# Kernel tuning notes

Measured on AMD Instinct MI355X. Metric: run time of the kernel, lower is better.

Reference implementation:

```python
import jax, jax.numpy as jnp
import numpy as np

B, D, H, Z, E = 65536, 128, 256, 128, 16  # batch, input, hidden, hyper, embedding


def setup_inputs() -> dict:
    key = jax.random.key(0)
    ks = jax.random.split(key, 20)
    s = 0.02  # small weight scale for numerical sanity
    return {
        "x": jax.random.normal(ks[0], (B, D), jnp.float32),
        "h0": jax.random.normal(ks[1], (B, H), jnp.float32),
        "c0": jax.random.normal(ks[2], (B, H), jnp.float32),
        "hhat0": jax.random.normal(ks[3], (B, Z), jnp.float32),
        "chat0": jax.random.normal(ks[4], (B, Z), jnp.float32),
        "hweight": jax.random.normal(ks[5], (Z + H + D, 4 * Z), jnp.float32) * s,
        "hbias": jnp.zeros((4 * Z,), jnp.float32),
        "zw_h": jax.random.normal(ks[6], (Z, 4 * E), jnp.float32) * s,
        "zw_x": jax.random.normal(ks[7], (Z, 4 * E), jnp.float32) * s,
        "zw_b": jax.random.normal(ks[8], (Z, 4 * E), jnp.float32) * 0.01,
        "zb_h": jnp.ones((4 * E,), jnp.float32),
        "zb_x": jnp.ones((4 * E,), jnp.float32),
        "dw_h": jnp.full((4, E, H), 0.1 / E, jnp.float32),  # [i,g,f,o] stacked
        "dw_x": jnp.full((4, E, H), 0.1 / E, jnp.float32),
        "dw_b": jax.random.normal(ks[9], (4, E, H), jnp.float32) * s,
        "weight": jax.random.normal(ks[10], (H + D, 4 * H), jnp.float32) * s,
        "bias": jnp.zeros((4 * H,), jnp.float32),
    }


def reference(x, h0, c0, hhat0, chat0, hweight, hbias, zw_h, zw_x, zw_b,
              zb_h, zb_x, dw_h, dw_x, dw_b, weight, bias):
    sig, tanh = jax.nn.sigmoid, jnp.tanh
    b = x.shape[0]
    # hyper LSTM cell
    gh = jnp.concatenate([hhat0, h0, x], axis=1) @ hweight + hbias  # [B, 4Z]
    i_h, g_h, f_h, o_h = jnp.split(gh, 4, axis=1)
    chat1 = sig(f_h) * chat0 + sig(i_h) * tanh(g_h)
    hhat1 = sig(o_h) * tanh(chat1)
    # embedding projections z (chunk order i,g,f,o -> reshape to [B,4,E])
    z_h = (hhat1 @ zw_h + zb_h).reshape(b, 4, E)
    z_x = (hhat1 @ zw_x + zb_x).reshape(b, 4, E)
    z_b = (hhat1 @ zw_b).reshape(b, 4, E)
    # d scaling vectors, [B,4,H] -> [B,4H]
    d_yh = jnp.einsum('bke,keh->bkh', z_h, dw_h).reshape(b, 4 * H)
    d_yx = jnp.einsum('bke,keh->bkh', z_x, dw_x).reshape(b, 4 * H)
    d_yb = jnp.einsum('bke,keh->bkh', z_b, dw_b).reshape(b, 4 * H)
    # main LSTM gates, hyper-modulated
    g = jnp.concatenate([h0, x], axis=1) @ weight * d_yh * d_yx + d_yb + bias
    i_g, g_g, f_g, o_g = jnp.split(g, 4, axis=1)
    c1 = sig(f_g) * c0 + sig(i_g) * tanh(g_g)
    h1 = sig(o_g) * tanh(c1)
    return (h1, c1, hhat1, chat1)
```

## Files before the change

kernel.cpp:

```cpp
#include <hip/hip_runtime.h>


typedef unsigned short u16;
typedef __attribute__((ext_vector_type(8))) short bf16x8;
typedef __attribute__((ext_vector_type(4))) float f32x4;

#define BATCH 65536

__device__ __forceinline__ u16 f2b(float f) {
  unsigned u = __float_as_uint(f);
  u += 0x7fffu + ((u >> 16) & 1u);
  return (u16)(u >> 16);
}
__device__ __forceinline__ unsigned pk2(float a, float b) {
  return (unsigned)f2b(a) | ((unsigned)f2b(b) << 16);
}
__device__ __forceinline__ float upk_lo(unsigned u) { return __uint_as_float(u << 16); }
__device__ __forceinline__ float upk_hi(unsigned u) { return __uint_as_float(u & 0xffff0000u); }
__device__ __forceinline__ float sigf(float x) { return 1.0f / (1.0f + __expf(-x)); }
__device__ __forceinline__ float tanhfast(float x) {
  float xc = fminf(fmaxf(x, -15.f), 15.f);
  float e = __expf(2.f * xc);
  return (e - 1.f) / (e + 1.f);
}
__device__ __forceinline__ int swz(int r, int c) { return r * 64 + (c ^ ((r & 7) << 3)); }

#define VM_BAR(N) do { \
  asm volatile("s_waitcnt vmcnt(" #N ")" ::: "memory"); \
  __builtin_amdgcn_s_barrier(); \
  __builtin_amdgcn_sched_barrier(0); } while (0)

__device__ __forceinline__ void gl_lds16(const u16* g, u16* l) {
  __builtin_amdgcn_global_load_lds(
      (const __attribute__((address_space(1))) void*)g,
      (__attribute__((address_space(3))) void*)l, 16, 0, 0);
}
__device__ __forceinline__ void stageA(const u16* base, int ldk, u16* lA, int t) {
  const int r = t >> 3, q = t & 7, wid = t >> 6;
  const int qs = (q ^ (r & 7)) << 3;
  gl_lds16(base + (size_t)r * ldk + qs, lA + wid * 512);
  gl_lds16(base + (size_t)(r + 32) * ldk + qs, lA + 2048 + wid * 512);
}

__global__ __launch_bounds__(256) void hlstm_pre(
    const float* __restrict__ hhat0, const float* __restrict__ h0,
    const float* __restrict__ x, u16* __restrict__ abuf,
    const float* __restrict__ hweight, const float* __restrict__ hbias,
    const float* __restrict__ zw_h, const float* __restrict__ zw_x, const float* __restrict__ zw_b,
    const float* __restrict__ zb_h, const float* __restrict__ zb_x,
    const float* __restrict__ dw_h, const float* __restrict__ dw_x, const float* __restrict__ dw_b,
    const float* __restrict__ weight, const float* __restrict__ bias,
    u16* __restrict__ hw_fr, float* __restrict__ hbias_r,
    u16* __restrict__ w_fr,  float* __restrict__ bias_r,
    u16* __restrict__ whp_fr, u16* __restrict__ wxp_fr, u16* __restrict__ wbp_fr,
    float* __restrict__ bhp_r, float* __restrict__ bxp_r)
{
  if (blockIdx.x < 4096) {
    const size_t stride = (size_t)4096 * 256;
    for (size_t i = (size_t)blockIdx.x * 256 + threadIdx.x;
         i < (size_t)BATCH * 64; i += stride) {
      const size_t b = i >> 6; const int c = (int)(i & 63);
      const float* src;
      if (c < 16)      src = hhat0 + b * 128 + c * 8;
      else if (c < 48) src = h0 + b * 256 + (size_t)(c - 16) * 8;
      else             src = x + b * 128 + (size_t)(c - 48) * 8;
      float4 v0 = ((const float4*)src)[0];
      float4 v1 = ((const float4*)src)[1];
      alignas(16) u16 o[8] = {f2b(v0.x), f2b(v0.y), f2b(v0.z), f2b(v0.w),
                              f2b(v1.x), f2b(v1.y), f2b(v1.z), f2b(v1.w)};
      *(uint4*)(abuf + i * 8) = *(const uint4*)o;
    }
    return;
  }
  const int tid = (blockIdx.x - 4096) * 256 + threadIdx.x;
  const int nt  = 512 * 256;

  for (int i = tid; i < 16 * 16384; i += nt) {
    int tile = i >> 14, r = i & 16383;
    int wc = r >> 12, h = (r >> 11) & 1, g = (r >> 9) & 3;
    int lane = (r >> 3) & 63, j = r & 7;
    int hb = tile >> 3, s = tile & 7;
    int k = s * 64 + h * 32 + (lane >> 4) * 8 + j;
    int col = g * 128 + hb * 64 + wc * 16 + (lane & 15);
    hw_fr[i] = f2b(hweight[k * 512 + col]);
  }
  for (int i = tid; i < 24 * 16384; i += nt) {
    int tile = i >> 14, r = i & 16383;
    int wc = r >> 12, h = (r >> 11) & 1, g = (r >> 9) & 3;
    int lane = (r >> 3) & 63, j = r & 7;
    int hb = tile / 6, s = tile % 6;
    int k = s * 64 + h * 32 + (lane >> 4) * 8 + j;
    int col = g * 256 + hb * 64 + wc * 16 + (lane & 15);
    w_fr[i] = f2b(weight[k * 1024 + col]);
  }
  for (int i = tid; i < 3 * 8 * 16384; i += nt) {
    int mat = i / (8 * 16384), rem = i % (8 * 16384);
    int tile = rem >> 14, r = rem & 16383;
    int wc = r >> 12, h = (r >> 11) & 1, g = (r >> 9) & 3;
    int lane = (r >> 3) & 63, j = r & 7;
    int hb = tile >> 1, s = tile & 1;
    int k = s * 64 + h * 32 + (lane >> 4) * 8 + j;
    int colh = hb * 64 + wc * 16 + (lane & 15);
    const float* zw = (mat == 0) ? zw_h : (mat == 1) ? zw_x : zw_b;
    const float* dw = (mat == 0) ? dw_h : (mat == 1) ? dw_x : dw_b;
    float sv = 0.f;
#pragma unroll
    for (int e = 0; e < 16; ++e)
      sv += zw[k * 64 + g * 16 + e] * dw[g * 4096 + e * 256 + colh];
    u16* dst = (mat == 0) ? whp_fr : (mat == 1) ? wxp_fr : wbp_fr;
    dst[rem] = f2b(sv);
  }
  for (int i = tid; i < 1024; i += nt) {
    int hb = i >> 8, g = (i >> 6) & 3, hh = i & 63;
    int h = hb * 64 + hh;
    float sh = 0.f, sx = 0.f;
#pragma unroll
    for (int e = 0; e < 16; ++e) {
      sh += zb_h[g * 16 + e] * dw_h[g * 4096 + e * 256 + h];
      sx += zb_x[g * 16 + e] * dw_x[g * 4096 + e * 256 + h];
    }
    bhp_r[i] = sh; bxp_r[i] = sx;
    bias_r[i] = bias[g * 256 + h];
  }
  for (int i = tid; i < 512; i += nt) {
    int gate = (i >> 6) & 3, hb = i >> 8, hh = i & 63;
    hbias_r[i] = hbias[gate * 128 + hb * 64 + hh];
  }
}

__global__ __launch_bounds__(256, 3) void hlstm_k1(
    const u16* __restrict__ abuf, const float* __restrict__ chat0,
    const u16* __restrict__ hw_fr, const float* __restrict__ hbias_r,
    float* __restrict__ d_out, u16* __restrict__ hbuf)
{
  __shared__ alignas(16) u16 lA[3][64 * 64];
  const int f = blockIdx.x;
  const int xcd = f & 7, s2 = f >> 3;
  const int rb = xcd * 128 + (s2 >> 1), hb = s2 & 1;
  const int t = threadIdx.x;
  const int lane = t & 63, wc = t >> 6;
  const int lr = lane & 15, kg = lane >> 4;

  f32x4 acc[4][4];
  const f32x4 zzero = {0.f, 0.f, 0.f, 0.f};
#pragma unroll
  for (int mf = 0; mf < 4; ++mf)
#pragma unroll
    for (int g = 0; g < 4; ++g) acc[mf][g] = zzero;

  const u16* arow = abuf + (size_t)rb * 64 * 512;

  bf16x8 breg[8];
  auto loadB = [&](const u16* bt) {
#pragma unroll
    for (int h = 0; h < 2; ++h)
#pragma unroll
      for (int g = 0; g < 4; ++g)
        breg[h * 4 + g] = *(const bf16x8*)&bt[((wc * 2 + h) * 4 + g) * 512 + lane * 8];
  };
  auto sweep = [&](f32x4 (&ac)[4][4], const u16* cA) {
#pragma unroll
    for (int h = 0; h < 2; ++h)
#pragma unroll
      for (int mf = 0; mf < 4; ++mf) {
        bf16x8 afr = *(const bf16x8*)&cA[swz(mf * 16 + lr, h * 32 + kg * 8)];
#pragma unroll
        for (int g = 0; g < 4; ++g)
          ac[mf][g] = __builtin_amdgcn_mfma_f32_16x16x32_bf16(afr, breg[h * 4 + g], ac[mf][g], 0, 0, 0);
      }
  };

  stageA(arow + 0 * 64, 512, lA[0], t);
  stageA(arow + 1 * 64, 512, lA[1], t);
  loadB(hw_fr + (size_t)(hb * 8 + 0) * 16384);
  VM_BAR(8);

#pragma unroll
  for (int ks = 0; ks < 8; ++ks) {
    if (ks < 6) stageA(arow + (ks + 2) * 64, 512, lA[(ks + 2) % 3], t);
    sweep(acc, lA[ks % 3]);
    if (ks < 7) loadB(hw_fr + (size_t)(hb * 8 + ks + 1) * 16384);
    if (ks < 6)       VM_BAR(10);
    else if (ks == 6) VM_BAR(8);
  }

  float hb4[4];
#pragma unroll
  for (int g = 0; g < 4; ++g) hb4[g] = hbias_r[hb * 256 + g * 64 + wc * 16 + lr];
  const int zc = hb * 64 + wc * 16 + lr;
  float* out_hh = d_out + (size_t)BATCH * 512;
  float* out_ch = d_out + (size_t)BATCH * 640;
#pragma unroll
  for (int mf = 0; mf < 4; ++mf)
#pragma unroll
    for (int r = 0; r < 4; ++r) {
      const int row = rb * 64 + mf * 16 + kg * 4 + r;
      const float gi = acc[mf][0][r] + hb4[0];
      const float gg = acc[mf][1][r] + hb4[1];
      const float gf = acc[mf][2][r] + hb4[2];
      const float go = acc[mf][3][r] + hb4[3];
      const float c0v = chat0[(size_t)row * 128 + zc];
      const float c1v = sigf(gf) * c0v + sigf(gi) * tanhfast(gg);
      const float h1v = sigf(go) * tanhfast(c1v);
      out_hh[(size_t)row * 128 + zc] = h1v;
      out_ch[(size_t)row * 128 + zc] = c1v;
      hbuf[(size_t)row * 128 + zc] = f2b(h1v);
    }
}

__global__ __launch_bounds__(256, 2) void hlstm_k2(
    const u16* __restrict__ abuf, const u16* __restrict__ hbuf,
    const float* __restrict__ c0,
    const u16* __restrict__ w_fr, const float* __restrict__ bias_r,
    const u16* __restrict__ whp_fr, const u16* __restrict__ wxp_fr, const u16* __restrict__ wbp_fr,
    const float* __restrict__ bhp_r, const float* __restrict__ bxp_r,
    float* __restrict__ d_out)
{
  __shared__ alignas(16) u16 lA[3][64 * 64];
  const int f = blockIdx.x;
  const int xcd = f & 7, s4 = f >> 3;
  const int rb = xcd * 128 + (s4 >> 2), hb = s4 & 3;
  const int t = threadIdx.x;
  const int lane = t & 63, wc = t >> 6;
  const int lr = lane & 15, kg = lane >> 4;

  const u16* amain = abuf + (size_t)rb * 64 * 512 + 128;
  const u16* ahyp  = hbuf + (size_t)rb * 64 * 128;

  auto aptr = [&](int s) -> const u16* {
    if (s >= 4 && s < 10) return amain + (s - 4) * 64;
    return ahyp + (s & 1) * 64;
  };
  auto aldk = [&](int s) -> int { return (s >= 4 && s < 10) ? 512 : 128; };
  auto bptr = [&](int s) -> const u16* {
    if (s < 2)  return whp_fr + (size_t)(hb * 2 + s) * 16384;
    if (s < 4)  return wxp_fr + (size_t)(hb * 2 + s - 2) * 16384;
    if (s < 10) return w_fr  + (size_t)(hb * 6 + s - 4) * 16384;
    return wbp_fr + (size_t)(hb * 2 + s - 10) * 16384;
  };

  f32x4 acc[4][4];
  const f32x4 zzero = {0.f, 0.f, 0.f, 0.f};
#pragma unroll
  for (int mf = 0; mf < 4; ++mf)
#pragma unroll
    for (int g = 0; g < 4; ++g) acc[mf][g] = zzero;

  unsigned dsc[4][4][2];

  bf16x8 breg[8];
  auto loadB = [&](const u16* bt) {
#pragma unroll
    for (int h = 0; h < 2; ++h)
#pragma unroll
      for (int g = 0; g < 4; ++g)
        breg[h * 4 + g] = *(const bf16x8*)&bt[((wc * 2 + h) * 4 + g) * 512 + lane * 8];
  };
  auto sweep = [&](f32x4 (&ac)[4][4], const u16* cA) {
#pragma unroll
    for (int h = 0; h < 2; ++h)
#pragma unroll
      for (int mf = 0; mf < 4; ++mf) {
        bf16x8 afr = *(const bf16x8*)&cA[swz(mf * 16 + lr, h * 32 + kg * 8)];
#pragma unroll
        for (int g = 0; g < 4; ++g)
          ac[mf][g] = __builtin_amdgcn_mfma_f32_16x16x32_bf16(afr, breg[h * 4 + g], ac[mf][g], 0, 0, 0);
      }
  };

  stageA(aptr(0), aldk(0), lA[0], t);
  stageA(aptr(1), aldk(1), lA[1], t);
  loadB(bptr(0));
  VM_BAR(8);

#pragma unroll
  for (int s = 0; s < 12; ++s) {
    if (s < 10) stageA(aptr(s + 2), aldk(s + 2), lA[(s + 2) % 3], t);
    if (s == 2 || s == 4) {
#pragma unroll
      for (int mf = 0; mf < 4; ++mf)
#pragma unroll
        for (int g = 0; g < 4; ++g) acc[mf][g] = zzero;
    }
    sweep(acc, lA[s % 3]);
    if (s < 11) loadB(bptr(s + 1));
    if (s == 1) {
      float bh4[4];
#pragma unroll
      for (int g = 0; g < 4; ++g) bh4[g] = bhp_r[hb * 256 + g * 64 + wc * 16 + lr];
#pragma unroll
      for (int mf = 0; mf < 4; ++mf)
#pragma unroll
        for (int g = 0; g < 4; ++g) {
          dsc[mf][g][0] = pk2(acc[mf][g][0] + bh4[g], acc[mf][g][1] + bh4[g]);
          dsc[mf][g][1] = pk2(acc[mf][g][2] + bh4[g], acc[mf][g][3] + bh4[g]);
        }
    } else if (s == 3) {
      float bx4[4];
#pragma unroll
      for (int g = 0; g < 4; ++g) bx4[g] = bxp_r[hb * 256 + g * 64 + wc * 16 + lr];
#pragma unroll
      for (int mf = 0; mf < 4; ++mf)
#pragma unroll
        for (int g = 0; g < 4; ++g) {
          float d0 = upk_lo(dsc[mf][g][0]) * (acc[mf][g][0] + bx4[g]);
          float d1 = upk_hi(dsc[mf][g][0]) * (acc[mf][g][1] + bx4[g]);
          float d2 = upk_lo(dsc[mf][g][1]) * (acc[mf][g][2] + bx4[g]);
          float d3 = upk_hi(dsc[mf][g][1]) * (acc[mf][g][3] + bx4[g]);
          dsc[mf][g][0] = pk2(d0, d1);
          dsc[mf][g][1] = pk2(d2, d3);
        }
    } else if (s == 9) {
#pragma unroll
      for (int mf = 0; mf < 4; ++mf)
#pragma unroll
        for (int g = 0; g < 4; ++g) {
          acc[mf][g][0] *= upk_lo(dsc[mf][g][0]);
          acc[mf][g][1] *= upk_hi(dsc[mf][g][0]);
          acc[mf][g][2] *= upk_lo(dsc[mf][g][1]);
          acc[mf][g][3] *= upk_hi(dsc[mf][g][1]);
        }
    }
    if (s < 10)       VM_BAR(10);
    else if (s == 10) VM_BAR(8);
  }

  const int hcol = hb * 64 + wc * 16 + lr;
  float b4[4];
#pragma unroll
  for (int g = 0; g < 4; ++g) b4[g] = bias_r[hb * 256 + g * 64 + wc * 16 + lr];
  float* out_c1 = d_out + (size_t)BATCH * 256;
#pragma unroll
  for (int mf = 0; mf < 4; ++mf)
#pragma unroll
    for (int r = 0; r < 4; ++r) {
      const int row = rb * 64 + mf * 16 + kg * 4 + r;
      const float gi = acc[mf][0][r] + b4[0];
      const float gg = acc[mf][1][r] + b4[1];
      const float gf = acc[mf][2][r] + b4[2];
      const float go = acc[mf][3][r] + b4[3];
      const float c0v = c0[(size_t)row * 256 + hcol];
      const float c1v = sigf(gf) * c0v + sigf(gi) * tanhfast(gg);
      const float h1v = sigf(go) * tanhfast(c1v);
      d_out[(size_t)row * 256 + hcol]  = h1v;
      out_c1[(size_t)row * 256 + hcol] = c1v;
    }
}

extern "C" void kernel_launch(void* const* d_in, const int* in_sizes, int n_in,
                              void* d_out, int out_size, void* d_ws, size_t ws_size,
                              hipStream_t stream)
{
  (void)in_sizes; (void)n_in; (void)out_size; (void)ws_size;
  const float* x       = (const float*)d_in[0];
  const float* h0      = (const float*)d_in[1];
  const float* c0      = (const float*)d_in[2];
  const float* hhat0   = (const float*)d_in[3];
  const float* chat0   = (const float*)d_in[4];
  const float* hweight = (const float*)d_in[5];
  const float* hbias   = (const float*)d_in[6];
  const float* zw_h    = (const float*)d_in[7];
  const float* zw_x    = (const float*)d_in[8];
  const float* zw_b    = (const float*)d_in[9];
  const float* zb_h    = (const float*)d_in[10];
  const float* zb_x    = (const float*)d_in[11];
  const float* dw_h    = (const float*)d_in[12];
  const float* dw_x    = (const float*)d_in[13];
  const float* dw_b    = (const float*)d_in[14];
  const float* weight  = (const float*)d_in[15];
  const float* bias    = (const float*)d_in[16];

  char* wsb = (char*)d_ws;
  u16*   abuf    = (u16*)(wsb + 0);
  u16*   hbuf    = (u16*)(wsb + 67108864);
  u16*   hw_fr   = (u16*)(wsb + 83886080);
  u16*   w_fr    = (u16*)(wsb + 84410368);
  u16*   whp_fr  = (u16*)(wsb + 85196800);
  u16*   wxp_fr  = (u16*)(wsb + 85458944);
  u16*   wbp_fr  = (u16*)(wsb + 85721088);
  float* hbias_r = (float*)(wsb + 85983232);
  float* bias_r  = (float*)(wsb + 85985280);
  float* bhp_r   = (float*)(wsb + 85989376);
  float* bxp_r   = (float*)(wsb + 85993472);

  hlstm_pre<<<dim3(4608), dim3(256), 0, stream>>>(
      hhat0, h0, x, abuf,
      hweight, hbias, zw_h, zw_x, zw_b, zb_h, zb_x, dw_h, dw_x, dw_b, weight, bias,
      hw_fr, hbias_r, w_fr, bias_r, whp_fr, wxp_fr, wbp_fr, bhp_r, bxp_r);

  hlstm_k1<<<dim3(2048), dim3(256), 0, stream>>>(
      abuf, chat0, hw_fr, hbias_r, (float*)d_out, hbuf);

  hlstm_k2<<<dim3(4096), dim3(256), 0, stream>>>(
      abuf, hbuf, c0, w_fr, bias_r, whp_fr, wxp_fr, wbp_fr, bhp_r, bxp_r, (float*)d_out);
}
```

Before: 273.6 us.

## Spill hyper scale vectors to LDS, double-buffer A, raise k2 occupancy

In the second kernel, the packed d-scale register array is moved into a per-thread LDS buffer, and the A staging drops from triple to double buffering, so each block needs fewer registers. Launch bounds go to three blocks per SIMD to raise occupancy. s_setprio is also wrapped around the MFMA sweeps in both kernels. The cost is a shallower prefetch pipeline with tighter wait barriers, extra LDS traffic, and more LDS per block (16KB A plus 32KB scales), which may itself cap occupancy.

Result: faster. 264.2 us (-3.4%).

```diff
diff --git a/kernel.cpp b/kernel.cpp
--- a/kernel.cpp
+++ b/kernel.cpp
@@ -159,6 +159,7 @@
         breg[h * 4 + g] = *(const bf16x8*)&bt[((wc * 2 + h) * 4 + g) * 512 + lane * 8];
   };
   auto sweep = [&](f32x4 (&ac)[4][4], const u16* cA) {
+    __builtin_amdgcn_s_setprio(1);
 #pragma unroll
     for (int h = 0; h < 2; ++h)
 #pragma unroll
@@ -168,6 +169,7 @@
         for (int g = 0; g < 4; ++g)
           ac[mf][g] = __builtin_amdgcn_mfma_f32_16x16x32_bf16(afr, breg[h * 4 + g], ac[mf][g], 0, 0, 0);
       }
+    __builtin_amdgcn_s_setprio(0);
   };
 
   stageA(arow + 0 * 64, 512, lA[0], t);
@@ -208,7 +210,7 @@
     }
 }
 
-__global__ __launch_bounds__(256, 2) void hlstm_k2(
+__global__ __launch_bounds__(256, 3) void hlstm_k2(
     const u16* __restrict__ abuf, const u16* __restrict__ hbuf,
     const float* __restrict__ c0,
     const u16* __restrict__ w_fr, const float* __restrict__ bias_r,
@@ -216,7 +218,8 @@
     const float* __restrict__ bhp_r, const float* __restrict__ bxp_r,
     float* __restrict__ d_out)
 {
-  __shared__ alignas(16) u16 lA[3][64 * 64];
+  __shared__ alignas(16) u16 lA[2][64 * 64];
+  __shared__ alignas(16) unsigned ldsc[8192];
   const int f = blockIdx.x;
   const int xcd = f & 7, s4 = f >> 3;
   const int rb = xcd * 128 + (s4 >> 2), hb = s4 & 3;
@@ -246,8 +249,6 @@
 #pragma unroll
     for (int g = 0; g < 4; ++g) acc[mf][g] = zzero;
 
-  unsigned dsc[4][4][2];
-
   bf16x8 breg[8];
   auto loadB = [&](const u16* bt) {
 #pragma unroll
@@ -257,6 +258,7 @@
         breg[h * 4 + g] = *(const bf16x8*)&bt[((wc * 2 + h) * 4 + g) * 512 + lane * 8];
   };
   auto sweep = [&](f32x4 (&ac)[4][4], const u16* cA) {
+    __builtin_amdgcn_s_setprio(1);
 #pragma unroll
     for (int h = 0; h < 2; ++h)
 #pragma unroll
@@ -266,24 +268,25 @@
         for (int g = 0; g < 4; ++g)
           ac[mf][g] = __builtin_amdgcn_mfma_f32_16x16x32_bf16(afr, breg[h * 4 + g], ac[mf][g], 0, 0, 0);
       }
+    __builtin_amdgcn_s_setprio(0);
   };
 
   stageA(aptr(0), aldk(0), lA[0], t);
-  stageA(aptr(1), aldk(1), lA[1], t);
   loadB(bptr(0));
   VM_BAR(8);
 
 #pragma unroll
   for (int s = 0; s < 12; ++s) {
-    if (s < 10) stageA(aptr(s + 2), aldk(s + 2), lA[(s + 2) % 3], t);
+    if (s < 11) stageA(aptr(s + 1), aldk(s + 1), lA[(s + 1) & 1], t);
     if (s == 2 || s == 4) {
 #pragma unroll
       for (int mf = 0; mf < 4; ++mf)
 #pragma unroll
         for (int g = 0; g < 4; ++g) acc[mf][g] = zzero;
     }
-    sweep(acc, lA[s % 3]);
+    sweep(acc, lA[s & 1]);
     if (s < 11) loadB(bptr(s + 1));
+
     if (s == 1) {
       float bh4[4];
 #pragma unroll
@@ -291,9 +294,14 @@
 #pragma unroll
       for (int mf = 0; mf < 4; ++mf)
 #pragma unroll
-        for (int g = 0; g < 4; ++g) {
-          dsc[mf][g][0] = pk2(acc[mf][g][0] + bh4[g], acc[mf][g][1] + bh4[g]);
-          dsc[mf][g][1] = pk2(acc[mf][g][2] + bh4[g], acc[mf][g][3] + bh4[g]);
+        for (int gp = 0; gp < 2; ++gp) {
+          const int g0 = gp * 2, g1 = gp * 2 + 1;
+          uint4 v;
+          v.x = pk2(acc[mf][g0][0] + bh4[g0], acc[mf][g0][1] + bh4[g0]);
+          v.y = pk2(acc[mf][g0][2] + bh4[g0], acc[mf][g0][3] + bh4[g0]);
+          v.z = pk2(acc[mf][g1][0] + bh4[g1], acc[mf][g1][1] + bh4[g1]);
+          v.w = pk2(acc[mf][g1][2] + bh4[g1], acc[mf][g1][3] + bh4[g1]);
+          *(uint4*)&ldsc[(mf * 2 + gp) * 1024 + t * 4] = v;
         }
     } else if (s == 3) {
       float bx4[4];
@@ -302,27 +310,37 @@
 #pragma unroll
       for (int mf = 0; mf < 4; ++mf)
 #pragma unroll
-        for (int g = 0; g < 4; ++g) {
-          float d0 = upk_lo(dsc[mf][g][0]) * (acc[mf][g][0] + bx4[g]);
-          float d1 = upk_hi(dsc[mf][g][0]) * (acc[mf][g][1] + bx4[g]);
-          float d2 = upk_lo(dsc[mf][g][1]) * (acc[mf][g][2] + bx4[g]);
-          float d3 = upk_hi(dsc[mf][g][1]) * (acc[mf][g][3] + bx4[g]);
-          dsc[mf][g][0] = pk2(d0, d1);
-          dsc[mf][g][1] = pk2(d2, d3);
+        for (int gp = 0; gp < 2; ++gp) {
+          const int g0 = gp * 2, g1 = gp * 2 + 1;
+          uint4 v = *(const uint4*)&ldsc[(mf * 2 + gp) * 1024 + t * 4];
+          v.x = pk2(upk_lo(v.x) * (acc[mf][g0][0] + bx4[g0]),
+                    upk_hi(v.x) * (acc[mf][g0][1] + bx4[g0]));
+          v.y = pk2(upk_lo(v.y) * (acc[mf][g0][2] + bx4[g0]),
+                    upk_hi(v.y) * (acc[mf][g0][3] + bx4[g0]));
+          v.z = pk2(upk_lo(v.z) * (acc[mf][g1][0] + bx4[g1]),
+                    upk_hi(v.z) * (acc[mf][g1][1] + bx4[g1]));
+          v.w = pk2(upk_lo(v.w) * (acc[mf][g1][2] + bx4[g1]),
+                    upk_hi(v.w) * (acc[mf][g1][3] + bx4[g1]));
+          *(uint4*)&ldsc[(mf * 2 + gp) * 1024 + t * 4] = v;
         }
     } else if (s == 9) {
 #pragma unroll
       for (int mf = 0; mf < 4; ++mf)
 #pragma unroll
-        for (int g = 0; g < 4; ++g) {
-          acc[mf][g][0] *= upk_lo(dsc[mf][g][0]);
-          acc[mf][g][1] *= upk_hi(dsc[mf][g][0]);
-          acc[mf][g][2] *= upk_lo(dsc[mf][g][1]);
-          acc[mf][g][3] *= upk_hi(dsc[mf][g][1]);
+        for (int gp = 0; gp < 2; ++gp) {
+          const int g0 = gp * 2, g1 = gp * 2 + 1;
+          uint4 v = *(const uint4*)&ldsc[(mf * 2 + gp) * 1024 + t * 4];
+          acc[mf][g0][0] *= upk_lo(v.x);
+          acc[mf][g0][1] *= upk_hi(v.x);
+          acc[mf][g0][2] *= upk_lo(v.y);
+          acc[mf][g0][3] *= upk_hi(v.y);
+          acc[mf][g1][0] *= upk_lo(v.z);
+          acc[mf][g1][1] *= upk_hi(v.z);
+          acc[mf][g1][2] *= upk_lo(v.w);
+          acc[mf][g1][3] *= upk_hi(v.w);
         }
     }
-    if (s < 10)       VM_BAR(10);
-    else if (s == 10) VM_BAR(8);
+    if (s < 11) VM_BAR(8);
   }
 
   const int hcol = hb * 64 + wc * 16 + lr;
```
